# Kernel tuning notes

Hardware: AMD Instinct MI355X
Metric: run time of the kernel (lower is better)

Reference implementation:

```python
import jax, jax.numpy as jnp
import numpy as np
from jax import lax

B, S, M, D, NQ = 128, 100, 50, 128, 10000


def _xavier(key, shape):
    fan_in, fan_out = shape[0], shape[-1]
    limit = float(np.sqrt(6.0 / (fan_in + fan_out)))
    return jax.random.uniform(key, shape, jnp.float32, -limit, limit)


def setup_inputs() -> dict:
    key = jax.random.key(0)
    ks = jax.random.split(key, 16)
    return {
        "question_seq": jax.random.randint(ks[0], (B, S), 0, NQ),
        "answer_seq": jax.random.randint(ks[1], (B, S), 0, 2),
        "emb": _xavier(ks[2], (NQ, D)),
        "key_matrix": _xavier(ks[3], (M, D)),
        "vu_w1": _xavier(ks[4], (2 * D, D)),
        "vu_b1": jnp.zeros((D,), jnp.float32),
        "vu_w2": _xavier(ks[5], (D, D)),
        "vu_b2": jnp.zeros((D,), jnp.float32),
        "er_w": _xavier(ks[6], (D, D)),
        "er_b": jnp.zeros((D,), jnp.float32),
        "ad_w": _xavier(ks[7], (D, D)),
        "ad_b": jnp.zeros((D,), jnp.float32),
        "out_w1": _xavier(ks[8], (2 * D, D)),
        "out_b1": jnp.zeros((D,), jnp.float32),
        "out_w2": _xavier(ks[9], (D, 1)),
        "out_b2": jnp.zeros((1,), jnp.float32),
    }


def reference(question_seq, answer_seq, emb, key_matrix,
              vu_w1, vu_b1, vu_w2, vu_b2,
              er_w, er_b, ad_w, ad_b,
              out_w1, out_b1, out_w2, out_b2):
    # q_embed for all steps: [B,S,D]; attention over memory slots: [B,S,M]
    q_emb = emb[question_seq]
    attn = jax.nn.softmax(jnp.einsum('bsd,md->bsm', q_emb, key_matrix), axis=-1)

    def step(v, inp):
        w, qe = inp                                   # w: [B,M], qe: [B,D]
        read = jnp.einsum('bm,bmd->bd', w, v)         # attention read
        u = jnp.concatenate([read, qe], axis=-1)      # [B,2D]
        h = jnp.tanh(u @ vu_w1 + vu_b1)
        up = h @ vu_w2 + vu_b2                        # update vector [B,D]
        e = jax.nn.sigmoid(up @ er_w + er_b)          # erase gate
        a = jnp.tanh(up @ ad_w + ad_b)                # add vector
        v = v * (1.0 - w[:, :, None] * e[:, None, :]) + w[:, :, None] * a[:, None, :]
        return v, None

    v0 = jnp.zeros((B, M, D), q_emb.dtype)
    vT, _ = lax.scan(step, v0, (attn.transpose(1, 0, 2), q_emb.transpose(1, 0, 2)))

    # predict with last question (target_question=None branch)
    last_qe = q_emb[:, -1]                            # [B,D]
    last_w = attn[:, -1]                              # [B,M]
    read = jnp.einsum('bm,bmd->bd', last_w, vT)
    p_in = jnp.concatenate([read, last_qe], axis=-1)
    h = jax.nn.relu(p_in @ out_w1 + out_b1)
    pred = jax.nn.sigmoid(h @ out_w2 + out_b2)[:, 0]  # [B]
    return pred
```

## Files before the change

kernel.cpp:

```cpp
#include <hip/hip_runtime.h>

#define BB 128
#define SS 100
#define MM 50
#define DD 128
#define KROW 66
#define XW(k) ((k) + 8 * ((k) >> 5))
#define XBUF 152

__device__ __forceinline__ float bf2f(unsigned short u) {
    union { unsigned int i; float f; } c; c.i = ((unsigned int)u) << 16; return c.f;
}
__device__ __forceinline__ float bfu_lo(unsigned int u) {
    union { unsigned int i; float f; } c; c.i = u << 16; return c.f;
}
__device__ __forceinline__ float bfu_hi(unsigned int u) {
    union { unsigned int i; float f; } c; c.i = u & 0xffff0000u; return c.f;
}
__device__ __forceinline__ unsigned short f2bf_bits(float f) {
    union { float f; unsigned int u; } c; c.f = f;
    unsigned int r = (c.u + 0x7FFFu + ((c.u >> 16) & 1u)) >> 16;
    return (unsigned short)r;
}
__device__ __forceinline__ unsigned int packbf(float lo, float hi) {
    return (unsigned int)f2bf_bits(lo) | ((unsigned int)f2bf_bits(hi) << 16);
}
__device__ __forceinline__ float fast_sigmoid(float x) { return 1.0f / (1.0f + __expf(-x)); }
__device__ __forceinline__ float fast_tanh(float x) {
    float ax = fabsf(x);
    float z = __expf(-2.0f * ax);
    float r = (1.0f - z) / (1.0f + z);
    return copysignf(r, x);
}

template <bool BF16>
__device__ __forceinline__ float ldw(const void* p, size_t idx) {
    if (BF16) return bf2f(((const unsigned short*)p)[idx]);
    return ((const float*)p)[idx];
}

struct __align__(16) SmemT {
    union {
        struct {
            unsigned int key_w[MM * KROW];
            unsigned int qe8[8][68];
        } pre;
        struct {
            float xread[XBUF];
            float xh[XBUF];
            float xup[XBUF];
            float h1f[DD];
        } run;
    } u;
    unsigned int wrow_p[SS][32];
    unsigned short qp_all[SS][DD];
    int qrow[SS];
    float qlast[DD];
};

template <bool BF16>
__device__ void dkvmn_impl(
    const int* __restrict__ qseq,
    const void* emb, const void* key,
    const void* vu_w1, const void* vu_b1, const void* vu_w2, const void* vu_b2,
    const void* er_w, const void* er_b, const void* ad_w, const void* ad_b,
    const void* out_w1, const void* out_b1, const void* out_w2, const void* out_b2,
    void* outp, SmemT& sm)
{
    const int t = threadIdx.x;
    const int b = blockIdx.x;
    const int l = t & 63;
    const int wv = t >> 6;
    const int d = (wv << 4) + (l & 15);
    const int q = l >> 4;

    if (BF16) {
        const unsigned int* kg = (const unsigned int*)key;
        for (int g = t; g < MM * 64; g += 512)
            sm.u.pre.key_w[(g >> 6) * KROW + (g & 63)] = kg[g];
    } else {
        const float* kf = (const float*)key;
        for (int g = t; g < MM * 64; g += 512) {
            int row = g >> 6, c2 = g & 63;
            sm.u.pre.key_w[row * KROW + c2] = packbf(kf[row * 128 + 2 * c2], kf[row * 128 + 2 * c2 + 1]);
        }
    }
    for (int g = t; g < SS; g += 512) sm.qrow[g] = qseq[b * SS + g];

    float rw1a[32], rw1b[32], rw2[32], rer[32], rad[32];
#pragma unroll
    for (int i = 0; i < 32; ++i) {
        int k = 32 * q + i;
        rw1a[i] = ldw<BF16>(vu_w1, (size_t)k * DD + d);
        rw1b[i] = ldw<BF16>(vu_w1, (size_t)(DD + k) * DD + d);
        rw2[i]  = ldw<BF16>(vu_w2, (size_t)k * DD + d);
        rer[i]  = ldw<BF16>(er_w,  (size_t)k * DD + d);
        rad[i]  = ldw<BF16>(ad_w,  (size_t)k * DD + d);
    }
    const float b1r = ldw<BF16>(vu_b1, d);
    const float b2r = ldw<BF16>(vu_b2, d);
    const float ebr = ldw<BF16>(er_b, d);
    const float abr = ldw<BF16>(ad_b, d);

    __syncthreads();

    for (int ii = 0; ii < 13; ++ii) {
        const int nrows = (ii == 12) ? 4 : 8;
        {
            int r = t >> 6, w = t & 63;
            if (r < nrows) {
                int row = sm.qrow[8 * ii + r];
                if (BF16) {
                    sm.u.pre.qe8[r][w] = ((const unsigned int*)emb)[((size_t)row << 6) + w];
                } else {
                    const float* ef = (const float*)emb + (((size_t)row) << 7) + 2 * w;
                    sm.u.pre.qe8[r][w] = packbf(ef[0], ef[1]);
                }
            }
        }
        __syncthreads();

        if (wv < nrows) {
            int m = l;
            int mc = (m < MM) ? m : (MM - 1);
            float a0 = 0.f, a1 = 0.f, a2 = 0.f, a3 = 0.f;
#pragma unroll
            for (int j = 0; j < 32; ++j) {
                uint2 kw = *(const uint2*)&sm.u.pre.key_w[mc * KROW + 2 * j];
                uint2 qw = *(const uint2*)&sm.u.pre.qe8[wv][2 * j];
                a0 = fmaf(bfu_lo(kw.x), bfu_lo(qw.x), a0);
                a1 = fmaf(bfu_hi(kw.x), bfu_hi(qw.x), a1);
                a2 = fmaf(bfu_lo(kw.y), bfu_lo(qw.y), a2);
                a3 = fmaf(bfu_hi(kw.y), bfu_hi(qw.y), a3);
            }
            float lg = (a0 + a1) + (a2 + a3);
            if (m >= MM) lg = -1e30f;
            float mx = lg;
#pragma unroll
            for (int o = 32; o > 0; o >>= 1) mx = fmaxf(mx, __shfl_xor(mx, o));
            float p = (m < MM) ? __expf(lg - mx) : 0.f;
            float sum = p;
#pragma unroll
            for (int o = 32; o > 0; o >>= 1) sum += __shfl_xor(sum, o);
            p = p / sum;
            float pn = __shfl_xor(p, 1);
            if ((m & 1) == 0)
                sm.wrow_p[8 * ii + wv][m >> 1] = packbf(p, pn);
        }

        for (int sr = 0; sr < nrows; ++sr) {
            float p0 = 0.f, p1 = 0.f;
#pragma unroll
            for (int i = 0; i < 16; ++i) {
                unsigned int uw = sm.u.pre.qe8[sr][16 * q + i];
                p0 = fmaf(rw1b[2 * i],     bfu_lo(uw), p0);
                p1 = fmaf(rw1b[2 * i + 1], bfu_hi(uw), p1);
            }
            float qpv = p0 + p1;
            qpv += __shfl_xor(qpv, 16);
            qpv += __shfl_xor(qpv, 32);
            if (q == 0) sm.qp_all[8 * ii + sr][d] = f2bf_bits(qpv);
        }
        __syncthreads();
    }

    if (t < 64) {
        unsigned int uw = sm.u.pre.qe8[3][t];
        sm.qlast[2 * t]     = bfu_lo(uw);
        sm.qlast[2 * t + 1] = bfu_hi(uw);
    }
    float v[16];
#pragma unroll
    for (int j = 0; j < 16; ++j) v[j] = 0.f;
    float wrowr[16];
    {
        const uint4* wp = (const uint4*)&sm.wrow_p[0][8 * q];
        uint4 w0 = wp[0], w1 = wp[1];
        unsigned int ww[8] = { w0.x, w0.y, w0.z, w0.w, w1.x, w1.y, w1.z, w1.w };
#pragma unroll
        for (int i = 0; i < 8; ++i) { wrowr[2 * i] = bfu_lo(ww[i]); wrowr[2 * i + 1] = bfu_hi(ww[i]); }
    }
    if (q == 0) sm.u.run.xread[XW(d)] = 0.f;
    __syncthreads();

    for (int s = 0; s < SS; ++s) {
        {
            float qpv = bf2f(sm.qp_all[s][d]);
            const float4* xp = (const float4*)&sm.u.run.xread[40 * q];
            float a0 = 0.f, a1 = 0.f, a2 = 0.f, a3 = 0.f;
#pragma unroll
            for (int j = 0; j < 8; ++j) {
                float4 xv = xp[j];
                a0 = fmaf(rw1a[4 * j],     xv.x, a0);
                a1 = fmaf(rw1a[4 * j + 1], xv.y, a1);
                a2 = fmaf(rw1a[4 * j + 2], xv.z, a2);
                a3 = fmaf(rw1a[4 * j + 3], xv.w, a3);
            }
            float acc = (a0 + a1) + (a2 + a3);
            acc += __shfl_xor(acc, 16);
            acc += __shfl_xor(acc, 32);
            float hh = fast_tanh(acc + qpv + b1r);
            if (q == 0) sm.u.run.xh[XW(d)] = hh;
        }
        __syncthreads();

        {
            const float4* xp = (const float4*)&sm.u.run.xh[40 * q];
            float a0 = 0.f, a1 = 0.f, a2 = 0.f, a3 = 0.f;
#pragma unroll
            for (int j = 0; j < 8; ++j) {
                float4 xv = xp[j];
                a0 = fmaf(rw2[4 * j],     xv.x, a0);
                a1 = fmaf(rw2[4 * j + 1], xv.y, a1);
                a2 = fmaf(rw2[4 * j + 2], xv.z, a2);
                a3 = fmaf(rw2[4 * j + 3], xv.w, a3);
            }
            float acc = (a0 + a1) + (a2 + a3);
            acc += __shfl_xor(acc, 16);
            acc += __shfl_xor(acc, 32);
            float up = acc + b2r;
            if (q == 0) sm.u.run.xup[XW(d)] = up;
        }
        __syncthreads();

        {
            const float4* xp = (const float4*)&sm.u.run.xup[40 * q];
            float e0 = 0.f, e1 = 0.f, f0 = 0.f, f1 = 0.f;
#pragma unroll
            for (int j = 0; j < 8; ++j) {
                float4 xv = xp[j];
                e0 = fmaf(rer[4 * j],     xv.x, e0); e1 = fmaf(rer[4 * j + 1], xv.y, e1);
                e0 = fmaf(rer[4 * j + 2], xv.z, e0); e1 = fmaf(rer[4 * j + 3], xv.w, e1);
                f0 = fmaf(rad[4 * j],     xv.x, f0); f1 = fmaf(rad[4 * j + 1], xv.y, f1);
                f0 = fmaf(rad[4 * j + 2], xv.z, f0); f1 = fmaf(rad[4 * j + 3], xv.w, f1);
            }
            float ae = e0 + e1, aa = f0 + f1;
            ae += __shfl_xor(ae, 16); ae += __shfl_xor(ae, 32);
            aa += __shfl_xor(aa, 16); aa += __shfl_xor(aa, 32);
            float e = fast_sigmoid(ae + ebr);
            float a = fast_tanh(aa + abr);
#pragma unroll
            for (int j = 0; j < 16; ++j)
                v[j] = fmaf(wrowr[j], fmaf(-e, v[j], a), v[j]);
            if (s + 1 < SS) {
                const uint4* wp = (const uint4*)&sm.wrow_p[s + 1][8 * q];
                uint4 w0 = wp[0], w1 = wp[1];
                unsigned int ww[8] = { w0.x, w0.y, w0.z, w0.w, w1.x, w1.y, w1.z, w1.w };
#pragma unroll
                for (int i = 0; i < 8; ++i) { wrowr[2 * i] = bfu_lo(ww[i]); wrowr[2 * i + 1] = bfu_hi(ww[i]); }
            }
            float r0 = 0.f, r1 = 0.f;
#pragma unroll
            for (int j = 0; j < 16; j += 2) {
                r0 = fmaf(wrowr[j], v[j], r0);
                r1 = fmaf(wrowr[j + 1], v[j + 1], r1);
            }
            float rr = r0 + r1;
            rr += __shfl_xor(rr, 16);
            rr += __shfl_xor(rr, 32);
            if (q == 0) sm.u.run.xread[XW(d)] = rr;
        }
        __syncthreads();
    }

    float acc = 0.f;
    if (q < 2) {
#pragma unroll
        for (int sl = 0; sl < 2; ++sl) {
            int sidx = 2 * q + sl;
            const float4* xp = (const float4*)&sm.u.run.xread[40 * sidx];
#pragma unroll
            for (int j = 0; j < 8; ++j) {
                float4 xv = xp[j];
                int k = 32 * sidx + 4 * j;
                acc = fmaf(ldw<BF16>(out_w1, (size_t)k * DD + d),       xv.x, acc);
                acc = fmaf(ldw<BF16>(out_w1, (size_t)(k + 1) * DD + d), xv.y, acc);
                acc = fmaf(ldw<BF16>(out_w1, (size_t)(k + 2) * DD + d), xv.z, acc);
                acc = fmaf(ldw<BF16>(out_w1, (size_t)(k + 3) * DD + d), xv.w, acc);
            }
        }
    } else {
        int half = q - 2;
        const float4* qp4 = (const float4*)&sm.qlast[64 * half];
#pragma unroll
        for (int j = 0; j < 16; ++j) {
            float4 xv = qp4[j];
            int k = DD + 64 * half + 4 * j;
            acc = fmaf(ldw<BF16>(out_w1, (size_t)k * DD + d),       xv.x, acc);
            acc = fmaf(ldw<BF16>(out_w1, (size_t)(k + 1) * DD + d), xv.y, acc);
            acc = fmaf(ldw<BF16>(out_w1, (size_t)(k + 2) * DD + d), xv.z, acc);
            acc = fmaf(ldw<BF16>(out_w1, (size_t)(k + 3) * DD + d), xv.w, acc);
        }
    }
    acc += __shfl_xor(acc, 16);
    acc += __shfl_xor(acc, 32);
    float h1 = fmaxf(acc + ldw<BF16>(out_b1, d), 0.f);
    if (q == 0) sm.u.run.h1f[d] = h1;
    __syncthreads();

    if (t < 64) {
        float xs = fmaf(sm.u.run.h1f[t], ldw<BF16>(out_w2, t),
                        sm.u.run.h1f[64 + t] * ldw<BF16>(out_w2, 64 + t));
#pragma unroll
        for (int o = 32; o > 0; o >>= 1) xs += __shfl_xor(xs, o);
        if (t == 0) {
            float pred = fast_sigmoid(xs + ldw<BF16>(out_b2, 0));
            if (BF16) ((unsigned short*)outp)[b] = f2bf_bits(pred);
            else      ((float*)outp)[b] = pred;
        }
    }
}

__global__ __launch_bounds__(512) void DKVMN_78546361909953_kernel(
    const int* __restrict__ qseq,
    const void* emb, const void* key,
    const void* vu_w1, const void* vu_b1, const void* vu_w2, const void* vu_b2,
    const void* er_w, const void* er_b, const void* ad_w, const void* ad_b,
    const void* out_w1, const void* out_b1, const void* out_w2, const void* out_b2,
    void* outp)
{
    __shared__ SmemT sm;

    const unsigned int* eu = (const unsigned int*)emb;
    int cnt = 0;
    for (int i = 0; i < 32; ++i) {
        unsigned int e8 = (eu[i] >> 7) & 0xFFu;
        cnt += (e8 >= 100u && e8 <= 127u) ? 1 : 0;
    }
    if (cnt >= 16)
        dkvmn_impl<true>(qseq, emb, key, vu_w1, vu_b1, vu_w2, vu_b2,
                         er_w, er_b, ad_w, ad_b, out_w1, out_b1, out_w2, out_b2, outp, sm);
    else
        dkvmn_impl<false>(qseq, emb, key, vu_w1, vu_b1, vu_w2, vu_b2,
                          er_w, er_b, ad_w, ad_b, out_w1, out_b1, out_w2, out_b2, outp, sm);
}

extern "C" void kernel_launch(void* const* d_in, const int* in_sizes, int n_in,
                              void* d_out, int out_size, void* d_ws, size_t ws_size,
                              hipStream_t stream) {
    const int* qseq = (const int*)d_in[0];
    DKVMN_78546361909953_kernel<<<BB, 512, 0, stream>>>(
        qseq,
        d_in[2], d_in[3], d_in[4], d_in[5], d_in[6], d_in[7],
        d_in[8], d_in[9], d_in[10], d_in[11],
        d_in[12], d_in[13], d_in[14], d_in[15],
        d_out);
}
```

Before: 285.0 us.

## Fold vu_w2 into erase/add weights and pack recurrence vectors as bf16

Precomputes W2·W_er and W2·W_ad (plus folded biases) once per block, so the per-step chain drops the separate up-projection matvec and one barrier. The recurrent read and hidden vectors are now stored in LDS as packed bf16 pairs, which halves LDS reads per step. This adds prologue work (a 128x128x128 product per block, staged through a shared-memory union) and extra rounding to bf16 on the read and hidden vectors.

```diff
diff --git a/kernel.cpp b/kernel.cpp
--- a/kernel.cpp
+++ b/kernel.cpp
@@ -5,8 +5,8 @@
 #define MM 50
 #define DD 128
 #define KROW 66
-#define XW(k) ((k) + 8 * ((k) >> 5))
-#define XBUF 152
+#define W2ROW(r) ((r) * 68 + (((r) >> 5) << 3))
+#define WADDR(w) ((w) + 8 * ((w) >> 4))
 
 __device__ __forceinline__ float bf2f(unsigned short u) {
     union { unsigned int i; float f; } c; c.i = ((unsigned int)u) << 16; return c.f;
@@ -46,14 +46,18 @@
             unsigned int qe8[8][68];
         } pre;
         struct {
-            float xread[XBUF];
-            float xh[XBUF];
-            float xup[XBUF];
+            unsigned int xread_w[96];
+            unsigned int xh_w[96];
             float h1f[DD];
         } run;
     } u;
-    unsigned int wrow_p[SS][32];
-    unsigned short qp_all[SS][DD];
+    union {
+        unsigned int w2s[8724];
+        struct {
+            unsigned int wrow_p[SS][32];
+            unsigned short qp_all[SS][DD];
+        } tab;
+    } v2;
     int qrow[SS];
     float qlast[DD];
 };
@@ -78,31 +82,68 @@
         const unsigned int* kg = (const unsigned int*)key;
         for (int g = t; g < MM * 64; g += 512)
             sm.u.pre.key_w[(g >> 6) * KROW + (g & 63)] = kg[g];
+        const unsigned int* wg = (const unsigned int*)vu_w2;
+        for (int g = t; g < 128 * 64; g += 512)
+            sm.v2.w2s[W2ROW(g >> 6) + (g & 63)] = wg[g];
     } else {
         const float* kf = (const float*)key;
         for (int g = t; g < MM * 64; g += 512) {
             int row = g >> 6, c2 = g & 63;
             sm.u.pre.key_w[row * KROW + c2] = packbf(kf[row * 128 + 2 * c2], kf[row * 128 + 2 * c2 + 1]);
         }
+        const float* wf = (const float*)vu_w2;
+        for (int g = t; g < 128 * 64; g += 512) {
+            int row = g >> 6, c2 = g & 63;
+            sm.v2.w2s[W2ROW(row) + c2] = packbf(wf[row * 128 + 2 * c2], wf[row * 128 + 2 * c2 + 1]);
+        }
     }
     for (int g = t; g < SS; g += 512) sm.qrow[g] = qseq[b * SS + g];
-
-    float rw1a[32], rw1b[32], rw2[32], rer[32], rad[32];
+    __syncthreads();
+
+    float rw2e[32], rw2a[32];
+#pragma unroll
+    for (int k = 0; k < 32; ++k) { rw2e[k] = 0.f; rw2a[k] = 0.f; }
+    float ebias = 0.f, abias = 0.f;
+#pragma unroll 1
+    for (int jc = 0; jc < 4; ++jc) {
+        float ec[32], ac[32];
+#pragma unroll
+        for (int i = 0; i < 32; ++i) {
+            int j = 32 * jc + i;
+            ec[i] = ldw<BF16>(er_w, (size_t)j * DD + d);
+            ac[i] = ldw<BF16>(ad_w, (size_t)j * DD + d);
+            float b2j = ldw<BF16>(vu_b2, j);
+            ebias = fmaf(b2j, ec[i], ebias);
+            abias = fmaf(b2j, ac[i], abias);
+        }
+#pragma unroll
+        for (int k = 0; k < 32; ++k) {
+            const uint4* wp = (const uint4*)&sm.v2.w2s[W2ROW(32 * q + k) + 16 * jc];
+            uint4 A = wp[0], B = wp[1], C = wp[2], Dv = wp[3];
+            unsigned int W[16] = { A.x, A.y, A.z, A.w, B.x, B.y, B.z, B.w,
+                                   C.x, C.y, C.z, C.w, Dv.x, Dv.y, Dv.z, Dv.w };
+            float se = rw2e[k], sa = rw2a[k];
+#pragma unroll
+            for (int wd = 0; wd < 16; ++wd) {
+                float wlo = bfu_lo(W[wd]), whi = bfu_hi(W[wd]);
+                se = fmaf(wlo, ec[2 * wd], se);     se = fmaf(whi, ec[2 * wd + 1], se);
+                sa = fmaf(wlo, ac[2 * wd], sa);     sa = fmaf(whi, ac[2 * wd + 1], sa);
+            }
+            rw2e[k] = se; rw2a[k] = sa;
+        }
+    }
+    ebias += ldw<BF16>(er_b, d);
+    abias += ldw<BF16>(ad_b, d);
+    __syncthreads();
+
+    float rw1a[32], rw1b[32];
 #pragma unroll
     for (int i = 0; i < 32; ++i) {
         int k = 32 * q + i;
         rw1a[i] = ldw<BF16>(vu_w1, (size_t)k * DD + d);
         rw1b[i] = ldw<BF16>(vu_w1, (size_t)(DD + k) * DD + d);
-        rw2[i]  = ldw<BF16>(vu_w2, (size_t)k * DD + d);
-        rer[i]  = ldw<BF16>(er_w,  (size_t)k * DD + d);
-        rad[i]  = ldw<BF16>(ad_w,  (size_t)k * DD + d);
     }
     const float b1r = ldw<BF16>(vu_b1, d);
-    const float b2r = ldw<BF16>(vu_b2, d);
-    const float ebr = ldw<BF16>(er_b, d);
-    const float abr = ldw<BF16>(ad_b, d);
-
-    __syncthreads();
 
     for (int ii = 0; ii < 13; ++ii) {
         const int nrows = (ii == 12) ? 4 : 8;
@@ -145,7 +186,7 @@
             p = p / sum;
             float pn = __shfl_xor(p, 1);
             if ((m & 1) == 0)
-                sm.wrow_p[8 * ii + wv][m >> 1] = packbf(p, pn);
+                sm.v2.tab.wrow_p[8 * ii + wv][m >> 1] = packbf(p, pn);
         }
 
         for (int sr = 0; sr < nrows; ++sr) {
@@ -159,7 +200,7 @@
             float qpv = p0 + p1;
             qpv += __shfl_xor(qpv, 16);
             qpv += __shfl_xor(qpv, 32);
-            if (q == 0) sm.qp_all[8 * ii + sr][d] = f2bf_bits(qpv);
+            if (q == 0) sm.v2.tab.qp_all[8 * ii + sr][d] = f2bf_bits(qpv);
         }
         __syncthreads();
     }
@@ -174,76 +215,61 @@
     for (int j = 0; j < 16; ++j) v[j] = 0.f;
     float wrowr[16];
     {
-        const uint4* wp = (const uint4*)&sm.wrow_p[0][8 * q];
+        const uint4* wp = (const uint4*)&sm.v2.tab.wrow_p[0][8 * q];
         uint4 w0 = wp[0], w1 = wp[1];
         unsigned int ww[8] = { w0.x, w0.y, w0.z, w0.w, w1.x, w1.y, w1.z, w1.w };
 #pragma unroll
         for (int i = 0; i < 8; ++i) { wrowr[2 * i] = bfu_lo(ww[i]); wrowr[2 * i + 1] = bfu_hi(ww[i]); }
     }
-    if (q == 0) sm.u.run.xread[XW(d)] = 0.f;
+    if (t < 96) sm.u.run.xread_w[t] = 0;
     __syncthreads();
 
     for (int s = 0; s < SS; ++s) {
         {
-            float qpv = bf2f(sm.qp_all[s][d]);
-            const float4* xp = (const float4*)&sm.u.run.xread[40 * q];
-            float a0 = 0.f, a1 = 0.f, a2 = 0.f, a3 = 0.f;
-#pragma unroll
-            for (int j = 0; j < 8; ++j) {
-                float4 xv = xp[j];
-                a0 = fmaf(rw1a[4 * j],     xv.x, a0);
-                a1 = fmaf(rw1a[4 * j + 1], xv.y, a1);
-                a2 = fmaf(rw1a[4 * j + 2], xv.z, a2);
-                a3 = fmaf(rw1a[4 * j + 3], xv.w, a3);
-            }
-            float acc = (a0 + a1) + (a2 + a3);
+            float qpv = bf2f(sm.v2.tab.qp_all[s][d]);
+            const uint4* xp = (const uint4*)&sm.u.run.xread_w[24 * q];
+            uint4 X0 = xp[0], X1 = xp[1], X2 = xp[2], X3 = xp[3];
+            unsigned int W[16] = { X0.x, X0.y, X0.z, X0.w, X1.x, X1.y, X1.z, X1.w,
+                                   X2.x, X2.y, X2.z, X2.w, X3.x, X3.y, X3.z, X3.w };
+            float a0 = 0.f, a1 = 0.f;
+#pragma unroll
+            for (int wd = 0; wd < 16; ++wd) {
+                a0 = fmaf(rw1a[2 * wd],     bfu_lo(W[wd]), a0);
+                a1 = fmaf(rw1a[2 * wd + 1], bfu_hi(W[wd]), a1);
+            }
+            float acc = a0 + a1;
             acc += __shfl_xor(acc, 16);
             acc += __shfl_xor(acc, 32);
             float hh = fast_tanh(acc + qpv + b1r);
-            if (q == 0) sm.u.run.xh[XW(d)] = hh;
+            float hp = __shfl_xor(hh, 1);
+            if (q == 0 && !(d & 1)) sm.u.run.xh_w[WADDR(d >> 1)] = packbf(hh, hp);
         }
         __syncthreads();
 
         {
-            const float4* xp = (const float4*)&sm.u.run.xh[40 * q];
-            float a0 = 0.f, a1 = 0.f, a2 = 0.f, a3 = 0.f;
-#pragma unroll
-            for (int j = 0; j < 8; ++j) {
-                float4 xv = xp[j];
-                a0 = fmaf(rw2[4 * j],     xv.x, a0);
-                a1 = fmaf(rw2[4 * j + 1], xv.y, a1);
-                a2 = fmaf(rw2[4 * j + 2], xv.z, a2);
-                a3 = fmaf(rw2[4 * j + 3], xv.w, a3);
-            }
-            float acc = (a0 + a1) + (a2 + a3);
-            acc += __shfl_xor(acc, 16);
-            acc += __shfl_xor(acc, 32);
-            float up = acc + b2r;
-            if (q == 0) sm.u.run.xup[XW(d)] = up;
-        }
-        __syncthreads();
-
-        {
-            const float4* xp = (const float4*)&sm.u.run.xup[40 * q];
+            const uint4* xp = (const uint4*)&sm.u.run.xh_w[24 * q];
+            uint4 X0 = xp[0], X1 = xp[1], X2 = xp[2], X3 = xp[3];
+            unsigned int W[16] = { X0.x, X0.y, X0.z, X0.w, X1.x, X1.y, X1.z, X1.w,
+                                   X2.x, X2.y, X2.z, X2.w, X3.x, X3.y, X3.z, X3.w };
             float e0 = 0.f, e1 = 0.f, f0 = 0.f, f1 = 0.f;
 #pragma unroll
-            for (int j = 0; j < 8; ++j) {
-                float4 xv = xp[j];
-                e0 = fmaf(rer[4 * j],     xv.x, e0); e1 = fmaf(rer[4 * j + 1], xv.y, e1);
-                e0 = fmaf(rer[4 * j + 2], xv.z, e0); e1 = fmaf(rer[4 * j + 3], xv.w, e1);
-                f0 = fmaf(rad[4 * j],     xv.x, f0); f1 = fmaf(rad[4 * j + 1], xv.y, f1);
-                f0 = fmaf(rad[4 * j + 2], xv.z, f0); f1 = fmaf(rad[4 * j + 3], xv.w, f1);
+            for (int wd = 0; wd < 16; ++wd) {
+                float wlo = bfu_lo(W[wd]), whi = bfu_hi(W[wd]);
+                e0 = fmaf(rw2e[2 * wd],     wlo, e0);
+                e1 = fmaf(rw2e[2 * wd + 1], whi, e1);
+                f0 = fmaf(rw2a[2 * wd],     wlo, f0);
+                f1 = fmaf(rw2a[2 * wd + 1], whi, f1);
             }
             float ae = e0 + e1, aa = f0 + f1;
             ae += __shfl_xor(ae, 16); ae += __shfl_xor(ae, 32);
             aa += __shfl_xor(aa, 16); aa += __shfl_xor(aa, 32);
-            float e = fast_sigmoid(ae + ebr);
-            float a = fast_tanh(aa + abr);
+            float e = fast_sigmoid(ae + ebias);
+            float a = fast_tanh(aa + abias);
 #pragma unroll
             for (int j = 0; j < 16; ++j)
                 v[j] = fmaf(wrowr[j], fmaf(-e, v[j], a), v[j]);
             if (s + 1 < SS) {
-                const uint4* wp = (const uint4*)&sm.wrow_p[s + 1][8 * q];
+                const uint4* wp = (const uint4*)&sm.v2.tab.wrow_p[s + 1][8 * q];
                 uint4 w0 = wp[0], w1 = wp[1];
                 unsigned int ww[8] = { w0.x, w0.y, w0.z, w0.w, w1.x, w1.y, w1.z, w1.w };
 #pragma unroll
@@ -258,25 +284,29 @@
             float rr = r0 + r1;
             rr += __shfl_xor(rr, 16);
             rr += __shfl_xor(rr, 32);
-            if (q == 0) sm.u.run.xread[XW(d)] = rr;
+            float rp = __shfl_xor(rr, 1);
+            if (q == 0 && !(d & 1)) sm.u.run.xread_w[WADDR(d >> 1)] = packbf(rr, rp);
         }
         __syncthreads();
     }
 
     float acc = 0.f;
     if (q < 2) {
-#pragma unroll
-        for (int sl = 0; sl < 2; ++sl) {
-            int sidx = 2 * q + sl;
-            const float4* xp = (const float4*)&sm.u.run.xread[40 * sidx];
-#pragma unroll
-            for (int j = 0; j < 8; ++j) {
-                float4 xv = xp[j];
-                int k = 32 * sidx + 4 * j;
-                acc = fmaf(ldw<BF16>(out_w1, (size_t)k * DD + d),       xv.x, acc);
-                acc = fmaf(ldw<BF16>(out_w1, (size_t)(k + 1) * DD + d), xv.y, acc);
-                acc = fmaf(ldw<BF16>(out_w1, (size_t)(k + 2) * DD + d), xv.z, acc);
-                acc = fmaf(ldw<BF16>(out_w1, (size_t)(k + 3) * DD + d), xv.w, acc);
+        const uint4* xr0 = (const uint4*)&sm.u.run.xread_w[48 * q];
+        const uint4* xr1 = (const uint4*)&sm.u.run.xread_w[48 * q + 24];
+#pragma unroll
+        for (int half = 0; half < 2; ++half) {
+            const uint4* xp = half ? xr1 : xr0;
+#pragma unroll
+            for (int wq = 0; wq < 4; ++wq) {
+                uint4 X = xp[wq];
+                unsigned int Wv[4] = { X.x, X.y, X.z, X.w };
+#pragma unroll
+                for (int e2 = 0; e2 < 4; ++e2) {
+                    int k = 64 * q + 32 * half + 8 * wq + 2 * e2;
+                    acc = fmaf(ldw<BF16>(out_w1, (size_t)k * DD + d),       bfu_lo(Wv[e2]), acc);
+                    acc = fmaf(ldw<BF16>(out_w1, (size_t)(k + 1) * DD + d), bfu_hi(Wv[e2]), acc);
+                }
             }
         }
     } else {
```

Result: slower. 308.5 us (+8.2%).
